# Optimization experiments

Hardware: AMD Instinct MI355X
Metric: run time of the kernel (lower is better)

Reference implementation:

```python
import jax, jax.numpy as jnp
import numpy as np

N, E, C = 50000, 600000, 128
H, O = 4, 32          # heads = C // 32, out_channels = 32, concat -> H*O == C
HO = H * O
EPS_LN = 1e-5


def _lin_init(key, fan_in, shape):
    return jax.random.normal(key, shape, dtype=jnp.float32) * (1.0 / np.sqrt(fan_in))


def setup_inputs() -> dict:
    key = jax.random.key(0)
    ks = jax.random.split(key, 16)
    return {
        "x": jax.random.normal(ks[0], (N, C), dtype=jnp.float32),
        "edge_attr": jax.random.normal(ks[1], (E, C), dtype=jnp.float32),
        "edge_index": jax.random.randint(ks[2], (2, E), 0, N, dtype=jnp.int64),
        # TransformerConv params
        "Wq": _lin_init(ks[3], C, (C, HO)), "bq": jnp.zeros((HO,), jnp.float32),
        "Wk": _lin_init(ks[4], C, (C, HO)), "bk": jnp.zeros((HO,), jnp.float32),
        "Wv": _lin_init(ks[5], C, (C, HO)), "bv": jnp.zeros((HO,), jnp.float32),
        "We": _lin_init(ks[6], C, (C, HO)),                      # lin_edge, no bias
        "Wskip": _lin_init(ks[7], C, (C, HO)), "bskip": jnp.zeros((HO,), jnp.float32),
        "Wbeta": _lin_init(ks[8], 3 * HO, (3 * HO,)),            # lin_beta, no bias
        # graph LayerNorms (affine)
        "g1": jnp.ones((C,), jnp.float32), "be1": jnp.zeros((C,), jnp.float32),
        "g2": jnp.ones((C,), jnp.float32), "be2": jnp.zeros((C,), jnp.float32),
        # FFN
        "W1": _lin_init(ks[9], C, (C, 4 * C)), "bf1": jnp.zeros((4 * C,), jnp.float32),
        "W2": _lin_init(ks[10], 4 * C, (4 * C, C)), "bf2": jnp.zeros((C,), jnp.float32),
    }


def _graph_ln(x, g, b):
    # PyG gnn.LayerNorm mode='graph', batch=None: scalar mean/std over ALL nodes+channels
    xm = x - jnp.mean(x)
    return (xm / (jnp.std(xm) + EPS_LN)) * g + b


def _transformer_conv(x, edge_index, edge_attr, Wq, bq, Wk, bk, Wv, bv, We,
                      Wskip, bskip, Wbeta):
    src, dst = edge_index[0], edge_index[1]   # flow source_to_target: i = dst
    q = (x @ Wq + bq).reshape(N, H, O)
    k = (x @ Wk + bk).reshape(N, H, O)
    v = (x @ Wv + bv).reshape(N, H, O)
    e = (edge_attr @ We).reshape(E, H, O)
    k_j = k[src] + e                           # [E,H,O]
    v_j = v[src] + e                           # [E,H,O]
    alpha = jnp.einsum('ehd,ehd->eh', q[dst], k_j) / np.sqrt(O)   # [E,H]
    # segment softmax over incoming edges of each target node
    m = jax.ops.segment_max(alpha, dst, num_segments=N)           # [N,H]
    a = jnp.exp(alpha - m[dst])
    s = jax.ops.segment_sum(a, dst, num_segments=N)               # [N,H]
    alpha = a / (s[dst] + 1e-16)
    out = jax.ops.segment_sum(alpha[..., None] * v_j, dst, num_segments=N)
    out = out.reshape(N, HO)
    # beta skip connection
    x_r = x @ Wskip + bskip
    beta = jax.nn.sigmoid(jnp.concatenate([out, x_r, out - x_r], axis=-1) @ Wbeta)
    beta = beta[:, None]
    return beta * x_r + (1.0 - beta) * out


def reference(x, edge_attr, edge_index, Wq, bq, Wk, bk, Wv, bv, We, Wskip, bskip,
              Wbeta, g1, be1, g2, be2, W1, bf1, W2, bf2):
    attn = _transformer_conv(x, edge_index, edge_attr, Wq, bq, Wk, bk, Wv, bv,
                             We, Wskip, bskip, Wbeta)
    x = _graph_ln(x + attn, g1, be1)
    ff = jax.nn.gelu(x @ W1 + bf1, approximate=False) @ W2 + bf2  # dropout: eval
    x = _graph_ln(x + ff, g2, be2)
    return x
```

## Files before the change

kernel.cpp:

```cpp
#include <hip/hip_runtime.h>
#include <math.h>

#define NN 50000
#define EE 600000
#define CD 128
#define FD 512
#define NCF 6400000.0

__device__ __forceinline__ float4 ld4(const float* p){ return *(const float4*)p; }

__global__ __launch_bounds__(256) void qkvs_gemm(
    const float* __restrict__ x,
    const float* __restrict__ Wq, const float* __restrict__ bq,
    const float* __restrict__ Wk, const float* __restrict__ bk,
    const float* __restrict__ Wv, const float* __restrict__ bv,
    const float* __restrict__ Wsk, const float* __restrict__ bsk,
    float* __restrict__ oq, float* __restrict__ okk,
    float* __restrict__ ov, float* __restrict__ osk)
{
    __shared__ float ast[32*132];
    __shared__ float bst[32*132];
    const int tid = threadIdx.x;
    const int r0 = blockIdx.x * 128;
    const float* W; const float* bias; float* out;
    switch (blockIdx.y) {
        case 0:  W = Wq;  bias = bq;  out = oq;  break;
        case 1:  W = Wk;  bias = bk;  out = okk; break;
        case 2:  W = Wv;  bias = bv;  out = ov;  break;
        default: W = Wsk; bias = bsk; out = osk; break;
    }
    const int tc = tid & 15, tr = tid >> 4;
    float acc[8][8];
    #pragma unroll
    for (int i = 0; i < 8; ++i)
        #pragma unroll
        for (int j = 0; j < 8; ++j) acc[i][j] = 0.f;

    for (int kc = 0; kc < 4; ++kc) {
        #pragma unroll
        for (int it = 0; it < 4; ++it) {
            int chunk = it*256 + tid;
            int row = chunk >> 3, c4 = chunk & 7;
            float4 g = make_float4(0.f,0.f,0.f,0.f);
            if (r0 + row < NN) g = ld4(&x[(r0+row)*CD + kc*32 + c4*4]);
            ast[(c4*4+0)*132 + row] = g.x;
            ast[(c4*4+1)*132 + row] = g.y;
            ast[(c4*4+2)*132 + row] = g.z;
            ast[(c4*4+3)*132 + row] = g.w;
        }
        #pragma unroll
        for (int it = 0; it < 4; ++it) {
            int chunk = it*256 + tid;
            int kr = chunk >> 5, c4 = chunk & 31;
            *(float4*)&bst[kr*132 + c4*4] = ld4(&W[(kc*32+kr)*CD + c4*4]);
        }
        __syncthreads();
        #pragma unroll
        for (int k = 0; k < 32; ++k) {
            float4 a0 = *(float4*)&ast[k*132 + tr*8];
            float4 a1 = *(float4*)&ast[k*132 + tr*8 + 4];
            float4 b0 = *(float4*)&bst[k*132 + tc*8];
            float4 b1 = *(float4*)&bst[k*132 + tc*8 + 4];
            float ar[8] = {a0.x,a0.y,a0.z,a0.w,a1.x,a1.y,a1.z,a1.w};
            float br[8] = {b0.x,b0.y,b0.z,b0.w,b1.x,b1.y,b1.z,b1.w};
            #pragma unroll
            for (int i = 0; i < 8; ++i)
                #pragma unroll
                for (int j = 0; j < 8; ++j)
                    acc[i][j] += ar[i]*br[j];
        }
        __syncthreads();
    }
    float bcol[8];
    #pragma unroll
    for (int j = 0; j < 8; ++j) bcol[j] = bias[tc*8+j];
    #pragma unroll
    for (int i = 0; i < 8; ++i) {
        int row = r0 + tr*8 + i;
        if (row < NN) {
            float4 o0 = make_float4(acc[i][0]+bcol[0], acc[i][1]+bcol[1],
                                    acc[i][2]+bcol[2], acc[i][3]+bcol[3]);
            float4 o1 = make_float4(acc[i][4]+bcol[4], acc[i][5]+bcol[5],
                                    acc[i][6]+bcol[6], acc[i][7]+bcol[7]);
            *(float4*)&out[row*CD + tc*8]     = o0;
            *(float4*)&out[row*CD + tc*8 + 4] = o1;
        }
    }
}

__global__ __launch_bounds__(256) void hist_kernel(const int* __restrict__ ei, int* __restrict__ cnt)
{
    int j = blockIdx.x*blockDim.x + threadIdx.x;
    if (j < EE) atomicAdd(&cnt[ei[EE + j]], 1);
}

__global__ __launch_bounds__(256) void scan_kernel(int* __restrict__ cnt, int* __restrict__ off)
{
    __shared__ int part[256];
    const int t = threadIdx.x;
    const int nper = (NN + 255) / 256;
    const int lo = t*nper, hi = min(lo + nper, NN);
    int ssum = 0;
    for (int i = lo; i < hi; ++i) ssum += cnt[i];
    part[t] = ssum;
    __syncthreads();
    if (t == 0) {
        int run = 0;
        for (int i = 0; i < 256; ++i) { int tmp = part[i]; part[i] = run; run += tmp; }
    }
    __syncthreads();
    int run = part[t];
    for (int i = lo; i < hi; ++i) {
        int c = cnt[i];
        off[i] = run;
        cnt[i] = run;
        run += c;
    }
    if (hi == NN) off[NN] = run;
}

__global__ __launch_bounds__(256) void scatter_kernel(
    const int* __restrict__ ei, int* __restrict__ cur, int* __restrict__ elist)
{
    int j = blockIdx.x*blockDim.x + threadIdx.x;
    if (j < EE) {
        int pos = atomicAdd(&cur[ei[EE + j]], 1);
        elist[pos] = j;
    }
}

__global__ __launch_bounds__(256) void alpha_kernel(
    const float* __restrict__ ea, const int* __restrict__ ei,
    const float* __restrict__ We,
    const float* __restrict__ q, const float* __restrict__ kmat,
    float* __restrict__ aout)
{
    __shared__ float ast[32*132];
    __shared__ float bst[32*132];
    __shared__ int sidx[128];
    __shared__ int didx[128];
    const int tid = threadIdx.x;
    const int e0 = blockIdx.x * 128;
    const int ne = min(128, EE - e0);
    if (tid < 128) {
        sidx[tid] = (tid < ne) ? ei[e0 + tid] : 0;
    } else {
        int le = tid - 128;
        didx[le] = (le < ne) ? ei[EE + e0 + le] : 0;
    }
    const int tc = tid & 15, tr = tid >> 4;
    float acc[8][8];
    #pragma unroll
    for (int i = 0; i < 8; ++i)
        #pragma unroll
        for (int j = 0; j < 8; ++j) acc[i][j] = 0.f;

    for (int kc = 0; kc < 4; ++kc) {
        #pragma unroll
        for (int it = 0; it < 4; ++it) {
            int chunk = it*256 + tid;
            int le = chunk >> 3, c4 = chunk & 7;
            float4 g = make_float4(0.f,0.f,0.f,0.f);
            if (le < ne) g = ld4(&ea[(size_t)(e0+le)*CD + kc*32 + c4*4]);
            ast[(c4*4+0)*132 + le] = g.x;
            ast[(c4*4+1)*132 + le] = g.y;
            ast[(c4*4+2)*132 + le] = g.z;
            ast[(c4*4+3)*132 + le] = g.w;
        }
        #pragma unroll
        for (int it = 0; it < 4; ++it) {
            int chunk = it*256 + tid;
            int kr = chunk >> 5, c4 = chunk & 31;
            *(float4*)&bst[kr*132 + c4*4] = ld4(&We[(kc*32+kr)*CD + c4*4]);
        }
        __syncthreads();
        #pragma unroll
        for (int k = 0; k < 32; ++k) {
            float4 a0 = *(float4*)&ast[k*132 + tr*8];
            float4 a1 = *(float4*)&ast[k*132 + tr*8 + 4];
            float4 b0 = *(float4*)&bst[k*132 + tc*8];
            float4 b1 = *(float4*)&bst[k*132 + tc*8 + 4];
            float ar[8] = {a0.x,a0.y,a0.z,a0.w,a1.x,a1.y,a1.z,a1.w};
            float br[8] = {b0.x,b0.y,b0.z,b0.w,b1.x,b1.y,b1.z,b1.w};
            #pragma unroll
            for (int i = 0; i < 8; ++i)
                #pragma unroll
                for (int j = 0; j < 8; ++j)
                    acc[i][j] += ar[i]*br[j];
        }
        __syncthreads();
    }
    const int head = tc >> 2;
    const float inv_sqrt_o = 0.17677669529663687f;
    #pragma unroll
    for (int i = 0; i < 8; ++i) {
        int le = tr*8 + i;
        if (le < ne) {
            int sn = sidx[le], dn = didx[le];
            const float* qp = q    + dn*CD + tc*8;
            const float* kp = kmat + sn*CD + tc*8;
            float4 qa = ld4(qp), qb = ld4(qp+4);
            float4 ka = ld4(kp), kb = ld4(kp+4);
            float p =
                qa.x*(ka.x+acc[i][0]) + qa.y*(ka.y+acc[i][1]) +
                qa.z*(ka.z+acc[i][2]) + qa.w*(ka.w+acc[i][3]) +
                qb.x*(kb.x+acc[i][4]) + qb.y*(kb.y+acc[i][5]) +
                qb.z*(kb.z+acc[i][6]) + qb.w*(kb.w+acc[i][7]);
            p += __shfl_xor(p, 1);
            p += __shfl_xor(p, 2);
            float a = expf(p * inv_sqrt_o);
            if ((tc & 3) == 0) aout[(size_t)(e0+le)*4 + head] = a;
        }
    }
}

__global__ __launch_bounds__(256) void node_kernel(
    const int* __restrict__ ei, const int* __restrict__ off, const int* __restrict__ elist,
    const float* __restrict__ a4, const float* __restrict__ ea,
    const float* __restrict__ vmat, const float* __restrict__ We,
    float* __restrict__ oa)
{
    __shared__ float s_lds[4][512];
    const int w = threadIdx.x >> 6;
    const int l = threadIdx.x & 63;
    const int n = blockIdx.x * 4 + w;
    if (n >= NN) return;
    const int beg = off[n], end = off[n+1];
    const int hsel = l >> 5;
    float s0k0=0,s1k0=0,s2k0=0,s3k0=0;
    float s0k1=0,s1k1=0,s2k1=0,s3k1=0;
    float av0=0, av1=0, den0=0, den1=0;
    for (int t = beg; t < end; ++t) {
        int eid = elist[t];
        int src = ei[eid];
        float4 aq = ld4(&a4[(size_t)eid*4]);
        float ea0 = ea[(size_t)eid*CD + l];
        float ea1 = ea[(size_t)eid*CD + 64 + l];
        float v0  = vmat[(size_t)src*CD + l];
        float v1  = vmat[(size_t)src*CD + 64 + l];
        float aH0 = hsel ? aq.y : aq.x;
        float aH1 = hsel ? aq.w : aq.z;
        s0k0 += aq.x*ea0; s1k0 += aq.y*ea0; s2k0 += aq.z*ea0; s3k0 += aq.w*ea0;
        s0k1 += aq.x*ea1; s1k1 += aq.y*ea1; s2k1 += aq.z*ea1; s3k1 += aq.w*ea1;
        av0 += aH0*v0; av1 += aH1*v1;
        den0 += aH0;   den1 += aH1;
    }
    s_lds[w][0*128 + l] = s0k0;  s_lds[w][0*128 + 64 + l] = s0k1;
    s_lds[w][1*128 + l] = s1k0;  s_lds[w][1*128 + 64 + l] = s1k1;
    s_lds[w][2*128 + l] = s2k0;  s_lds[w][2*128 + 64 + l] = s2k1;
    s_lds[w][3*128 + l] = s3k0;  s_lds[w][3*128 + 64 + l] = s3k1;
    const float* sh0 = &s_lds[w][hsel*128];
    const float* sh1 = &s_lds[w][(2+hsel)*128];
    float oe0 = 0.f, oe1 = 0.f;
    #pragma unroll 4
    for (int k = 0; k < 128; ++k) {
        float w0 = We[k*CD + l];
        float w1 = We[k*CD + 64 + l];
        oe0 += sh0[k] * w0;
        oe1 += sh1[k] * w1;
    }
    oa[(size_t)n*CD + l]      = (av0 + oe0) / (den0 + 1e-16f);
    oa[(size_t)n*CD + 64 + l] = (av1 + oe1) / (den1 + 1e-16f);
}

__global__ __launch_bounds__(256) void combine_kernel(
    const float* __restrict__ x, const float* __restrict__ xr,
    const float* __restrict__ oa,
    const float* __restrict__ Wbeta, float* __restrict__ y, double* __restrict__ red)
{
    const int lane = threadIdx.x & 63;
    const int wid = blockIdx.x*4 + (threadIdx.x >> 6);
    const int nw = gridDim.x*4;
    const int c0 = lane, c1 = lane + 64;
    const float wb_o0 = Wbeta[c0],     wb_o1 = Wbeta[c1];
    const float wb_x0 = Wbeta[128+c0], wb_x1 = Wbeta[128+c1];
    const float wb_d0 = Wbeta[256+c0], wb_d1 = Wbeta[256+c1];
    float lsum = 0.f, lsq = 0.f;
    for (int n = wid; n < NN; n += nw) {
        float o0 = oa[n*CD+c0];
        float o1 = oa[n*CD+c1];
        float r0v = xr[n*CD+c0], r1v = xr[n*CD+c1];
        float d = o0*wb_o0 + r0v*wb_x0 + (o0-r0v)*wb_d0
                + o1*wb_o1 + r1v*wb_x1 + (o1-r1v)*wb_d1;
        #pragma unroll
        for (int off = 32; off; off >>= 1) d += __shfl_xor(d, off);
        float beta = 1.0f / (1.0f + expf(-d));
        float y0 = x[n*CD+c0] + beta*r0v + (1.0f-beta)*o0;
        float y1 = x[n*CD+c1] + beta*r1v + (1.0f-beta)*o1;
        y[n*CD+c0] = y0; y[n*CD+c1] = y1;
        lsum += y0 + y1; lsq += y0*y0 + y1*y1;
    }
    #pragma unroll
    for (int off = 32; off; off >>= 1) {
        lsum += __shfl_xor(lsum, off);
        lsq  += __shfl_xor(lsq,  off);
    }
    if (lane == 0) {
        atomicAdd(&red[0], (double)lsum);
        atomicAdd(&red[1], (double)lsq);
    }
}

__global__ __launch_bounds__(256) void ffn1_gemm(
    const float* __restrict__ y, const float* __restrict__ W1, const float* __restrict__ bf1,
    const float* __restrict__ lng, const float* __restrict__ lnb,
    const double* __restrict__ red, float* __restrict__ h)
{
    __shared__ float ast[32*132];
    __shared__ float bst[32*132];
    const int tid = threadIdx.x;
    const int r0 = blockIdx.x * 128;
    const int cb = blockIdx.y;
    double m = red[0] * (1.0/NCF);
    double var = red[1] * (1.0/NCF) - m*m;
    if (var < 0.0) var = 0.0;
    const float mean = (float)m;
    const float scale = (float)(1.0 / (sqrt(var) + 1e-5));
    const int tc = tid & 15, tr = tid >> 4;
    float acc[8][8];
    #pragma unroll
    for (int i = 0; i < 8; ++i)
        #pragma unroll
        for (int j = 0; j < 8; ++j) acc[i][j] = 0.f;

    for (int kc = 0; kc < 4; ++kc) {
        #pragma unroll
        for (int it = 0; it < 4; ++it) {
            int chunk = it*256 + tid;
            int row = chunk >> 3, c4 = chunk & 7;
            float4 g = make_float4(0.f,0.f,0.f,0.f);
            if (r0 + row < NN) g = ld4(&y[(r0+row)*CD + kc*32 + c4*4]);
            int col = kc*32 + c4*4;
            g.x = (g.x - mean)*scale*lng[col+0] + lnb[col+0];
            g.y = (g.y - mean)*scale*lng[col+1] + lnb[col+1];
            g.z = (g.z - mean)*scale*lng[col+2] + lnb[col+2];
            g.w = (g.w - mean)*scale*lng[col+3] + lnb[col+3];
            ast[(c4*4+0)*132 + row] = g.x;
            ast[(c4*4+1)*132 + row] = g.y;
            ast[(c4*4+2)*132 + row] = g.z;
            ast[(c4*4+3)*132 + row] = g.w;
        }
        #pragma unroll
        for (int it = 0; it < 4; ++it) {
            int chunk = it*256 + tid;
            int kr = chunk >> 5, c4 = chunk & 31;
            *(float4*)&bst[kr*132 + c4*4] = ld4(&W1[(size_t)(kc*32+kr)*FD + cb*128 + c4*4]);
        }
        __syncthreads();
        #pragma unroll
        for (int k = 0; k < 32; ++k) {
            float4 a0 = *(float4*)&ast[k*132 + tr*8];
            float4 a1 = *(float4*)&ast[k*132 + tr*8 + 4];
            float4 b0 = *(float4*)&bst[k*132 + tc*8];
            float4 b1 = *(float4*)&bst[k*132 + tc*8 + 4];
            float ar[8] = {a0.x,a0.y,a0.z,a0.w,a1.x,a1.y,a1.z,a1.w};
            float br[8] = {b0.x,b0.y,b0.z,b0.w,b1.x,b1.y,b1.z,b1.w};
            #pragma unroll
            for (int i = 0; i < 8; ++i)
                #pragma unroll
                for (int j = 0; j < 8; ++j)
                    acc[i][j] += ar[i]*br[j];
        }
        __syncthreads();
    }
    float bcol[8];
    #pragma unroll
    for (int j = 0; j < 8; ++j) bcol[j] = bf1[cb*128 + tc*8 + j];
    #pragma unroll
    for (int i = 0; i < 8; ++i) {
        int row = r0 + tr*8 + i;
        if (row < NN) {
            float o[8];
            #pragma unroll
            for (int j = 0; j < 8; ++j) {
                float hv = acc[i][j] + bcol[j];
                o[j] = 0.5f*hv*(1.0f + erff(hv*0.7071067811865476f));
            }
            float4 o0 = make_float4(o[0],o[1],o[2],o[3]);
            float4 o1 = make_float4(o[4],o[5],o[6],o[7]);
            *(float4*)&h[(size_t)row*FD + cb*128 + tc*8]     = o0;
            *(float4*)&h[(size_t)row*FD + cb*128 + tc*8 + 4] = o1;
        }
    }
}

__global__ __launch_bounds__(256) void ffn2_gemm(
    const float* __restrict__ h, const float* __restrict__ W2, const float* __restrict__ bf2,
    const float* __restrict__ y, const float* __restrict__ lng, const float* __restrict__ lnb,
    double* __restrict__ red, float* __restrict__ outz)
{
    __shared__ float ast[32*132];
    __shared__ float bst[32*132];
    const int tid = threadIdx.x;
    const int r0 = blockIdx.x * 128;
    double m = red[0] * (1.0/NCF);
    double var = red[1] * (1.0/NCF) - m*m;
    if (var < 0.0) var = 0.0;
    const float mean = (float)m;
    const float scale = (float)(1.0 / (sqrt(var) + 1e-5));
    const int tc = tid & 15, tr = tid >> 4;
    float acc[8][8];
    #pragma unroll
    for (int i = 0; i < 8; ++i)
        #pragma unroll
        for (int j = 0; j < 8; ++j) acc[i][j] = 0.f;

    for (int kc = 0; kc < 16; ++kc) {
        #pragma unroll
        for (int it = 0; it < 4; ++it) {
            int chunk = it*256 + tid;
            int row = chunk >> 3, c4 = chunk & 7;
            float4 g = make_float4(0.f,0.f,0.f,0.f);
            if (r0 + row < NN) g = ld4(&h[(size_t)(r0+row)*FD + kc*32 + c4*4]);
            ast[(c4*4+0)*132 + row] = g.x;
            ast[(c4*4+1)*132 + row] = g.y;
            ast[(c4*4+2)*132 + row] = g.z;
            ast[(c4*4+3)*132 + row] = g.w;
        }
        #pragma unroll
        for (int it = 0; it < 4; ++it) {
            int chunk = it*256 + tid;
            int kr = chunk >> 5, c4 = chunk & 31;
            *(float4*)&bst[kr*132 + c4*4] = ld4(&W2[(size_t)(kc*32+kr)*CD + c4*4]);
        }
        __syncthreads();
        #pragma unroll
        for (int k = 0; k < 32; ++k) {
            float4 a0 = *(float4*)&ast[k*132 + tr*8];
            float4 a1 = *(float4*)&ast[k*132 + tr*8 + 4];
            float4 b0 = *(float4*)&bst[k*132 + tc*8];
            float4 b1 = *(float4*)&bst[k*132 + tc*8 + 4];
            float ar[8] = {a0.x,a0.y,a0.z,a0.w,a1.x,a1.y,a1.z,a1.w};
            float br[8] = {b0.x,b0.y,b0.z,b0.w,b1.x,b1.y,b1.z,b1.w};
            #pragma unroll
            for (int i = 0; i < 8; ++i)
                #pragma unroll
                for (int j = 0; j < 8; ++j)
                    acc[i][j] += ar[i]*br[j];
        }
        __syncthreads();
    }
    float g1c[8], b1c[8], bfc[8];
    #pragma unroll
    for (int j = 0; j < 8; ++j) {
        int col = tc*8 + j;
        g1c[j] = lng[col]; b1c[j] = lnb[col]; bfc[j] = bf2[col];
    }
    float lsum = 0.f, lsq = 0.f;
    #pragma unroll
    for (int i = 0; i < 8; ++i) {
        int row = r0 + tr*8 + i;
        if (row < NN) {
            float4 ya = ld4(&y[row*CD + tc*8]);
            float4 yb = ld4(&y[row*CD + tc*8 + 4]);
            float yv[8] = {ya.x,ya.y,ya.z,ya.w,yb.x,yb.y,yb.z,yb.w};
            float z[8];
            #pragma unroll
            for (int j = 0; j < 8; ++j) {
                float x1 = (yv[j] - mean)*scale*g1c[j] + b1c[j];
                z[j] = acc[i][j] + bfc[j] + x1;
                lsum += z[j]; lsq += z[j]*z[j];
            }
            float4 z0 = make_float4(z[0],z[1],z[2],z[3]);
            float4 z1 = make_float4(z[4],z[5],z[6],z[7]);
            *(float4*)&outz[row*CD + tc*8]     = z0;
            *(float4*)&outz[row*CD + tc*8 + 4] = z1;
        }
    }
    #pragma unroll
    for (int off = 32; off; off >>= 1) {
        lsum += __shfl_xor(lsum, off);
        lsq  += __shfl_xor(lsq,  off);
    }
    if ((threadIdx.x & 63) == 0) {
        atomicAdd(&red[2], (double)lsum);
        atomicAdd(&red[3], (double)lsq);
    }
}

__global__ __launch_bounds__(256) void ln2_kernel(
    float* __restrict__ z, const float* __restrict__ g2, const float* __restrict__ b2,
    const double* __restrict__ red)
{
    double m = red[2] * (1.0/NCF);
    double var = red[3] * (1.0/NCF) - m*m;
    if (var < 0.0) var = 0.0;
    const float mean = (float)m;
    const float scale = (float)(1.0 / (sqrt(var) + 1e-5));
    const int stride = gridDim.x * blockDim.x;
    for (int i = blockIdx.x*blockDim.x + threadIdx.x; i < NN*32; i += stride) {
        int c4 = (i & 31) * 4;
        float4 zv = *(float4*)&z[(size_t)i*4];
        float4 gv = ld4(&g2[c4]);
        float4 bv = ld4(&b2[c4]);
        zv.x = (zv.x - mean)*scale*gv.x + bv.x;
        zv.y = (zv.y - mean)*scale*gv.y + bv.y;
        zv.z = (zv.z - mean)*scale*gv.z + bv.z;
        zv.w = (zv.w - mean)*scale*gv.w + bv.w;
        *(float4*)&z[(size_t)i*4] = zv;
    }
}

extern "C" void kernel_launch(void* const* d_in, const int* in_sizes, int n_in,
                              void* d_out, int out_size, void* d_ws, size_t ws_size,
                              hipStream_t stream) {
    const float* x     = (const float*)d_in[0];
    const float* ea    = (const float*)d_in[1];
    const int*   ei    = (const int*)d_in[2];
    const float* Wq    = (const float*)d_in[3];
    const float* bq    = (const float*)d_in[4];
    const float* Wk    = (const float*)d_in[5];
    const float* bk    = (const float*)d_in[6];
    const float* Wv    = (const float*)d_in[7];
    const float* bv    = (const float*)d_in[8];
    const float* We    = (const float*)d_in[9];
    const float* Wsk   = (const float*)d_in[10];
    const float* bsk   = (const float*)d_in[11];
    const float* Wbeta = (const float*)d_in[12];
    const float* g1v   = (const float*)d_in[13];
    const float* be1   = (const float*)d_in[14];
    const float* g2v   = (const float*)d_in[15];
    const float* be2   = (const float*)d_in[16];
    const float* W1    = (const float*)d_in[17];
    const float* bf1   = (const float*)d_in[18];
    const float* W2    = (const float*)d_in[19];
    const float* bf2   = (const float*)d_in[20];

    float* wsf = (float*)d_ws;
    float* q    = wsf;
    float* kk   = wsf +  6400000;
    float* vv   = wsf + 12800000;
    float* xr   = wsf + 19200000;
    float* oa   = wsf + 25600000;
    float* a4   = wsf + 32000000;
    int*   off  = (int*)(wsf + 34400000);
    int*   cur  = off + 50001;
    int*   elist= cur + 50000;
    double* red = (double*)(wsf + 35100056);
    float* y = q;
    float* h = kk;
    float* zout = (float*)d_out;

    (void)hipMemsetAsync(cur, 0, 50000*sizeof(int), stream);
    (void)hipMemsetAsync(red, 0, 4*sizeof(double), stream);

    hist_kernel<<<(EE+255)/256, 256, 0, stream>>>(ei, cur);
    scan_kernel<<<1, 256, 0, stream>>>(cur, off);
    scatter_kernel<<<(EE+255)/256, 256, 0, stream>>>(ei, cur, elist);

    dim3 gA((NN + 127)/128, 4);
    qkvs_gemm<<<gA, 256, 0, stream>>>(x, Wq,bq, Wk,bk, Wv,bv, Wsk,bsk, q, kk, vv, xr);

    alpha_kernel<<<(EE + 127)/128, 256, 0, stream>>>(ea, ei, We, q, kk, a4);

    node_kernel<<<(NN + 3)/4, 256, 0, stream>>>(ei, off, elist, a4, ea, vv, We, oa);

    combine_kernel<<<1024, 256, 0, stream>>>(x, xr, oa, Wbeta, y, red);

    dim3 gF((NN + 127)/128, 4);
    ffn1_gemm<<<gF, 256, 0, stream>>>(y, W1, bf1, g1v, be1, red, h);

    ffn2_gemm<<<(NN + 127)/128, 256, 0, stream>>>(h, W2, bf2, y, g1v, be1, red, zout);

    ln2_kernel<<<2048, 256, 0, stream>>>(zout, g2v, be2, red);
}
```

Measured before the change: 1.614 ms.

## Fuse edge-score computation into per-node attention kernel via projected query

Removes the separate alpha kernel, which ran a per-edge GEMM of edge_attr with We and stored exp scores. The node kernel now projects each destination's query through We once (wq = We·q per head), so edge scores become a dot product of edge_attr with wq plus q·k[src]. These are reduced across the wavefront with shuffles and exponentiated inline. This avoids the 600k×128×128 edge GEMM and the a4 round trip through memory. In exchange, each edge iteration in the gather loop does four 6-step wavefront reductions plus an extra k gather, which adds latency to the serial per-node loop.

```diff
diff --git a/kernel.cpp b/kernel.cpp
--- a/kernel.cpp
+++ b/kernel.cpp
@@ -129,135 +129,96 @@
     }
 }
 
-__global__ __launch_bounds__(256) void alpha_kernel(
-    const float* __restrict__ ea, const int* __restrict__ ei,
-    const float* __restrict__ We,
-    const float* __restrict__ q, const float* __restrict__ kmat,
-    float* __restrict__ aout)
-{
-    __shared__ float ast[32*132];
-    __shared__ float bst[32*132];
-    __shared__ int sidx[128];
-    __shared__ int didx[128];
-    const int tid = threadIdx.x;
-    const int e0 = blockIdx.x * 128;
-    const int ne = min(128, EE - e0);
-    if (tid < 128) {
-        sidx[tid] = (tid < ne) ? ei[e0 + tid] : 0;
-    } else {
-        int le = tid - 128;
-        didx[le] = (le < ne) ? ei[EE + e0 + le] : 0;
-    }
-    const int tc = tid & 15, tr = tid >> 4;
-    float acc[8][8];
-    #pragma unroll
-    for (int i = 0; i < 8; ++i)
-        #pragma unroll
-        for (int j = 0; j < 8; ++j) acc[i][j] = 0.f;
-
-    for (int kc = 0; kc < 4; ++kc) {
-        #pragma unroll
-        for (int it = 0; it < 4; ++it) {
-            int chunk = it*256 + tid;
-            int le = chunk >> 3, c4 = chunk & 7;
-            float4 g = make_float4(0.f,0.f,0.f,0.f);
-            if (le < ne) g = ld4(&ea[(size_t)(e0+le)*CD + kc*32 + c4*4]);
-            ast[(c4*4+0)*132 + le] = g.x;
-            ast[(c4*4+1)*132 + le] = g.y;
-            ast[(c4*4+2)*132 + le] = g.z;
-            ast[(c4*4+3)*132 + le] = g.w;
-        }
-        #pragma unroll
-        for (int it = 0; it < 4; ++it) {
-            int chunk = it*256 + tid;
-            int kr = chunk >> 5, c4 = chunk & 31;
-            *(float4*)&bst[kr*132 + c4*4] = ld4(&We[(kc*32+kr)*CD + c4*4]);
-        }
-        __syncthreads();
-        #pragma unroll
-        for (int k = 0; k < 32; ++k) {
-            float4 a0 = *(float4*)&ast[k*132 + tr*8];
-            float4 a1 = *(float4*)&ast[k*132 + tr*8 + 4];
-            float4 b0 = *(float4*)&bst[k*132 + tc*8];
-            float4 b1 = *(float4*)&bst[k*132 + tc*8 + 4];
-            float ar[8] = {a0.x,a0.y,a0.z,a0.w,a1.x,a1.y,a1.z,a1.w};
-            float br[8] = {b0.x,b0.y,b0.z,b0.w,b1.x,b1.y,b1.z,b1.w};
-            #pragma unroll
-            for (int i = 0; i < 8; ++i)
-                #pragma unroll
-                for (int j = 0; j < 8; ++j)
-                    acc[i][j] += ar[i]*br[j];
-        }
-        __syncthreads();
-    }
-    const int head = tc >> 2;
-    const float inv_sqrt_o = 0.17677669529663687f;
-    #pragma unroll
-    for (int i = 0; i < 8; ++i) {
-        int le = tr*8 + i;
-        if (le < ne) {
-            int sn = sidx[le], dn = didx[le];
-            const float* qp = q    + dn*CD + tc*8;
-            const float* kp = kmat + sn*CD + tc*8;
-            float4 qa = ld4(qp), qb = ld4(qp+4);
-            float4 ka = ld4(kp), kb = ld4(kp+4);
-            float p =
-                qa.x*(ka.x+acc[i][0]) + qa.y*(ka.y+acc[i][1]) +
-                qa.z*(ka.z+acc[i][2]) + qa.w*(ka.w+acc[i][3]) +
-                qb.x*(kb.x+acc[i][4]) + qb.y*(kb.y+acc[i][5]) +
-                qb.z*(kb.z+acc[i][6]) + qb.w*(kb.w+acc[i][7]);
-            p += __shfl_xor(p, 1);
-            p += __shfl_xor(p, 2);
-            float a = expf(p * inv_sqrt_o);
-            if ((tc & 3) == 0) aout[(size_t)(e0+le)*4 + head] = a;
-        }
-    }
-}
-
-__global__ __launch_bounds__(256) void node_kernel(
+__global__ __launch_bounds__(256) void fused_attn_kernel(
     const int* __restrict__ ei, const int* __restrict__ off, const int* __restrict__ elist,
-    const float* __restrict__ a4, const float* __restrict__ ea,
-    const float* __restrict__ vmat, const float* __restrict__ We,
-    float* __restrict__ oa)
-{
-    __shared__ float s_lds[4][512];
+    const float* __restrict__ ea, const float* __restrict__ q,
+    const float* __restrict__ kmat, const float* __restrict__ vmat,
+    const float* __restrict__ We, float* __restrict__ oa)
+{
+    __shared__ float lds[4][640];
     const int w = threadIdx.x >> 6;
     const int l = threadIdx.x & 63;
-    const int n = blockIdx.x * 4 + w;
+    const int n = blockIdx.x*4 + w;
     if (n >= NN) return;
+    float* qs = &lds[w][0];
+    float* ss = &lds[w][128];
+    const int hsel = l >> 5;
+
+    float q0 = q[(size_t)n*CD + l];
+    float q1 = q[(size_t)n*CD + 64 + l];
+    qs[l] = q0;
+    qs[64 + l] = q1;
+
+    const float* Wr0 = We + (size_t)l*CD;
+    const float* Wr1 = We + (size_t)(64+l)*CD;
+    float wq[4][2];
+    #pragma unroll
+    for (int h = 0; h < 4; ++h) {
+        float a0 = 0.f, a1 = 0.f;
+        #pragma unroll
+        for (int d4 = 0; d4 < 8; ++d4) {
+            float4 qv = *(float4*)&qs[h*32 + d4*4];
+            float4 w0 = ld4(&Wr0[h*32 + d4*4]);
+            float4 w1 = ld4(&Wr1[h*32 + d4*4]);
+            a0 += w0.x*qv.x + w0.y*qv.y + w0.z*qv.z + w0.w*qv.w;
+            a1 += w1.x*qv.x + w1.y*qv.y + w1.z*qv.z + w1.w*qv.w;
+        }
+        wq[h][0] = a0; wq[h][1] = a1;
+    }
+
     const int beg = off[n], end = off[n+1];
-    const int hsel = l >> 5;
-    float s0k0=0,s1k0=0,s2k0=0,s3k0=0;
-    float s0k1=0,s1k1=0,s2k1=0,s3k1=0;
+    const float inv_sqrt_o = 0.17677669529663687f;
+    float s00=0,s01=0,s10=0,s11=0,s20=0,s21=0,s30=0,s31=0;
     float av0=0, av1=0, den0=0, den1=0;
     for (int t = beg; t < end; ++t) {
         int eid = elist[t];
         int src = ei[eid];
-        float4 aq = ld4(&a4[(size_t)eid*4]);
         float ea0 = ea[(size_t)eid*CD + l];
         float ea1 = ea[(size_t)eid*CD + 64 + l];
+        float k0  = kmat[(size_t)src*CD + l];
+        float k1  = kmat[(size_t)src*CD + 64 + l];
         float v0  = vmat[(size_t)src*CD + l];
         float v1  = vmat[(size_t)src*CD + 64 + l];
-        float aH0 = hsel ? aq.y : aq.x;
-        float aH1 = hsel ? aq.w : aq.z;
-        s0k0 += aq.x*ea0; s1k0 += aq.y*ea0; s2k0 += aq.z*ea0; s3k0 += aq.w*ea0;
-        s0k1 += aq.x*ea1; s1k1 += aq.y*ea1; s2k1 += aq.z*ea1; s3k1 += aq.w*ea1;
-        av0 += aH0*v0; av1 += aH1*v1;
-        den0 += aH0;   den1 += aH1;
-    }
-    s_lds[w][0*128 + l] = s0k0;  s_lds[w][0*128 + 64 + l] = s0k1;
-    s_lds[w][1*128 + l] = s1k0;  s_lds[w][1*128 + 64 + l] = s1k1;
-    s_lds[w][2*128 + l] = s2k0;  s_lds[w][2*128 + 64 + l] = s2k1;
-    s_lds[w][3*128 + l] = s3k0;  s_lds[w][3*128 + 64 + l] = s3k1;
-    const float* sh0 = &s_lds[w][hsel*128];
-    const float* sh1 = &s_lds[w][(2+hsel)*128];
+        float p0 = ea0*wq[0][0] + ea1*wq[0][1];
+        float p1 = ea0*wq[1][0] + ea1*wq[1][1];
+        float p2 = ea0*wq[2][0] + ea1*wq[2][1];
+        float p3 = ea0*wq[3][0] + ea1*wq[3][1];
+        float qkL = q0*k0;
+        float qkH = q1*k1;
+        if (hsel == 0) { p0 += qkL; p2 += qkH; }
+        else           { p1 += qkL; p3 += qkH; }
+        #pragma unroll
+        for (int o = 32; o; o >>= 1) {
+            p0 += __shfl_xor(p0, o);
+            p1 += __shfl_xor(p1, o);
+            p2 += __shfl_xor(p2, o);
+            p3 += __shfl_xor(p3, o);
+        }
+        float aH0 = expf(p0 * inv_sqrt_o);
+        float aH1 = expf(p1 * inv_sqrt_o);
+        float aH2 = expf(p2 * inv_sqrt_o);
+        float aH3 = expf(p3 * inv_sqrt_o);
+        s00 += aH0*ea0; s01 += aH0*ea1;
+        s10 += aH1*ea0; s11 += aH1*ea1;
+        s20 += aH2*ea0; s21 += aH2*ea1;
+        s30 += aH3*ea0; s31 += aH3*ea1;
+        float aL = hsel ? aH1 : aH0;
+        float aH = hsel ? aH3 : aH2;
+        av0 += aL*v0; av1 += aH*v1;
+        den0 += aL;   den1 += aH;
+    }
+
+    ss[0*128 + l] = s00;  ss[0*128 + 64 + l] = s01;
+    ss[1*128 + l] = s10;  ss[1*128 + 64 + l] = s11;
+    ss[2*128 + l] = s20;  ss[2*128 + 64 + l] = s21;
+    ss[3*128 + l] = s30;  ss[3*128 + 64 + l] = s31;
+    const float* sh0 = &ss[hsel*128];
+    const float* sh1 = &ss[(2+hsel)*128];
     float oe0 = 0.f, oe1 = 0.f;
     #pragma unroll 4
     for (int k = 0; k < 128; ++k) {
-        float w0 = We[k*CD + l];
-        float w1 = We[k*CD + 64 + l];
-        oe0 += sh0[k] * w0;
-        oe1 += sh1[k] * w1;
+        oe0 += sh0[k] * We[k*CD + l];
+        oe1 += sh1[k] * We[k*CD + 64 + l];
     }
     oa[(size_t)n*CD + l]      = (av0 + oe0) / (den0 + 1e-16f);
     oa[(size_t)n*CD + 64 + l] = (av1 + oe1) / (den1 + 1e-16f);
@@ -532,7 +493,6 @@
     float* vv   = wsf + 12800000;
     float* xr   = wsf + 19200000;
     float* oa   = wsf + 25600000;
-    float* a4   = wsf + 32000000;
     int*   off  = (int*)(wsf + 34400000);
     int*   cur  = off + 50001;
     int*   elist= cur + 50000;
@@ -551,9 +511,7 @@
     dim3 gA((NN + 127)/128, 4);
     qkvs_gemm<<<gA, 256, 0, stream>>>(x, Wq,bq, Wk,bk, Wv,bv, Wsk,bsk, q, kk, vv, xr);
 
-    alpha_kernel<<<(EE + 127)/128, 256, 0, stream>>>(ea, ei, We, q, kk, a4);
-
-    node_kernel<<<(NN + 3)/4, 256, 0, stream>>>(ei, off, elist, a4, ea, vv, We, oa);
+    fused_attn_kernel<<<(NN + 3)/4, 256, 0, stream>>>(ei, off, elist, ea, q, kk, vv, We, oa);
 
     combine_kernel<<<1024, 256, 0, stream>>>(x, xr, oa, Wbeta, y, red);
 
```

Result: slower. 1.933 ms (+19.8%).
